# Optimization experiments

Hardware: AMD Instinct MI355X
Metric: run time of the kernel (lower is better)

The kernel has to match this reference:

```python
import jax, jax.numpy as jnp
import numpy as np

N_NODES = 50000
N_INC = 300000
IN_DIM = 256
OUT_DIM = 256
NEG_SLOPE = 0.2
BN_EPS = 1e-5


def setup_inputs() -> dict:
    key = jax.random.key(0)
    ks = jax.random.split(key, 8)
    x = jax.random.normal(ks[0], (N_NODES, IN_DIM), dtype=jnp.float32)
    node_idx = jax.random.randint(ks[1], (N_INC,), 0, N_NODES)
    edge_idx = jax.random.randint(ks[2], (N_INC,), 0, 20000)
    W = jax.random.normal(ks[3], (IN_DIM, OUT_DIM), dtype=jnp.float32) / np.sqrt(IN_DIM)
    att = jax.random.normal(ks[4], (2 * OUT_DIM,), dtype=jnp.float32) * 0.1
    bias = jnp.zeros((OUT_DIM,), dtype=jnp.float32)
    gamma = jnp.ones((OUT_DIM,), dtype=jnp.float32)
    beta = jnp.zeros((OUT_DIM,), dtype=jnp.float32)
    return {
        'x': x, 'node_idx': node_idx, 'edge_idx': edge_idx,
        'num_hyperedges': 20000,
        'W': W, 'att': att, 'bias': bias, 'gamma': gamma, 'beta': beta,
    }


def reference(x, node_idx, edge_idx, num_hyperedges, W, att, bias, gamma, beta):
    N = x.shape[0]
    M = num_hyperedges
    xw = x @ W                                  # [N, D]

    # attention over incidences (old-PyG: edge feature := node feature at edge id)
    x_i = xw[node_idx]                          # [E, D]
    x_j = xw[edge_idx]                          # [E, D]
    alpha = jnp.sum(jnp.concatenate([x_i, x_j], axis=-1) * att, axis=-1)  # [E]
    alpha = jax.nn.leaky_relu(alpha, NEG_SLOPE)
    # segment softmax grouped by node index
    amax = jax.ops.segment_max(alpha, node_idx, num_segments=N)
    amax = jnp.where(jnp.isfinite(amax), amax, 0.0)
    e = jnp.exp(alpha - amax[node_idx])
    esum = jax.ops.segment_sum(e, node_idx, num_segments=N)
    alpha = e / (esum[node_idx] + 1e-16)        # [E]

    ones = jnp.ones_like(alpha)
    Dn = jax.ops.segment_sum(ones, node_idx, num_segments=N)   # node degree
    Dinv = jnp.where(Dn > 0, 1.0 / Dn, 0.0)
    Be = jax.ops.segment_sum(ones, edge_idx, num_segments=M)   # edge degree
    Binv = jnp.where(Be > 0, 1.0 / Be, 0.0)

    # stage 1: node -> hyperedge, norm = B at target edge
    msg1 = (Binv[edge_idx] * alpha)[:, None] * x_i              # [E, D]
    edge_feat = jax.ops.segment_sum(msg1, edge_idx, num_segments=M)  # [M, D]

    # stage 2: hyperedge -> node, norm = D at target node
    msg2 = (Dinv[node_idx] * alpha)[:, None] * edge_feat[edge_idx]   # [E, D]
    out = jax.ops.segment_sum(msg2, node_idx, num_segments=N) + bias  # [N, D]

    # BatchNorm1d (training: batch stats, biased variance) + ELU
    mu = jnp.mean(out, axis=0)
    var = jnp.mean((out - mu) ** 2, axis=0)
    out = gamma * (out - mu) * jax.lax.rsqrt(var + BN_EPS) + beta
    return jax.nn.elu(out)
```

## Files before the change

### kernel.cpp

```cpp
#include <hip/hip_runtime.h>

#define N_NODES 50000
#define N_INC   300000
#define DIM     256
#define M_EDGES 20000
#define NEG_SLOPE 0.2f
#define BN_EPS  1e-5f
#define EBLK 20
#define NBLK 49

typedef __attribute__((ext_vector_type(8))) short short8;
typedef __attribute__((ext_vector_type(4))) float f32x4;

__device__ __forceinline__ unsigned bf16rn(float f) {
    unsigned u = __float_as_uint(f);
    return (u + 0x7FFFu + ((u >> 16) & 1u)) >> 16;
}
__device__ __forceinline__ float4 unp4(uint2 p) {
    return make_float4(__uint_as_float(p.x << 16),
                       __uint_as_float(p.x & 0xFFFF0000u),
                       __uint_as_float(p.y << 16),
                       __uint_as_float(p.y & 0xFFFF0000u));
}

__global__ void wt_kernel(const float* __restrict__ W, ushort* __restrict__ WT)
{
    int i = blockIdx.x * 256 + threadIdx.x;
    int k = i >> 8, n = i & 255;
    WT[n * 256 + k] = (ushort)bf16rn(W[i]);
}

#define GBM 256
__global__ __launch_bounds__(512) void gemm_persist(
    const float* __restrict__ A, const ushort* __restrict__ WT,
    const float* __restrict__ att,
    ushort* __restrict__ xwb, float* __restrict__ s1, float* __restrict__ s2)
{
    __shared__ __align__(16) char Bs[131072];
    int tid = threadIdx.x;
    int lane = tid & 63, w = tid >> 6;

    #pragma unroll
    for (int i = 0; i < 16; ++i) {
        int flat = tid + 512 * i;
        int n = flat >> 5, kc = flat & 31;
        uint4 v = *(const uint4*)(WT + n * 256 + kc * 8);
        int off = n * 512 + ((kc * 16) ^ ((n & 7) << 4));
        *(uint4*)(Bs + off) = v;
    }
    __syncthreads();

    int row0 = blockIdx.x * GBM + w * 32;

    short8 afrag[2][8];
    #pragma unroll
    for (int j = 0; j < 8; ++j) {
        #pragma unroll
        for (int s = 0; s < 2; ++s) {
            int row = row0 + s * 16 + (lane & 15);
            float4 u0 = make_float4(0.f, 0.f, 0.f, 0.f), u1 = u0;
            if (row < N_NODES) {
                const float* p = A + (size_t)row * DIM + j * 32 + (lane >> 4) * 8;
                u0 = *(const float4*)p;
                u1 = *(const float4*)(p + 4);
            }
            uint4 q;
            q.x = bf16rn(u0.x) | (bf16rn(u0.y) << 16);
            q.y = bf16rn(u0.z) | (bf16rn(u0.w) << 16);
            q.z = bf16rn(u1.x) | (bf16rn(u1.y) << 16);
            q.w = bf16rn(u1.z) | (bf16rn(u1.w) << 16);
            afrag[s][j] = *(short8*)&q;
        }
    }

    float p1a[2][4] = {}, p2a[2][4] = {};
    #pragma unroll
    for (int ch = 0; ch < 2; ++ch) {
        f32x4 acc[2][8] = {};
        #pragma unroll
        for (int j = 0; j < 8; ++j) {
            int kb = j * 64 + (lane >> 4) * 16;
            #pragma unroll
            for (int c = 0; c < 8; ++c) {
                int col = ch * 128 + c * 16 + (lane & 15);
                short8 b = *(const short8*)(Bs + col * 512 + (kb ^ ((col & 7) << 4)));
                acc[0][c] = __builtin_amdgcn_mfma_f32_16x16x32_bf16(afrag[0][j], b, acc[0][c], 0, 0, 0);
                acc[1][c] = __builtin_amdgcn_mfma_f32_16x16x32_bf16(afrag[1][j], b, acc[1][c], 0, 0, 0);
            }
        }
        #pragma unroll
        for (int c = 0; c < 8; ++c) {
            int col = ch * 128 + c * 16 + (lane & 15);
            float a1 = att[col], a2 = att[DIM + col];
            #pragma unroll
            for (int s = 0; s < 2; ++s)
                #pragma unroll
                for (int r = 0; r < 4; ++r) {
                    int row = row0 + s * 16 + (lane >> 4) * 4 + r;
                    float v = acc[s][c][r];
                    if (row < N_NODES)
                        xwb[(size_t)row * DIM + col] = (ushort)bf16rn(v);
                    p1a[s][r] += v * a1;
                    p2a[s][r] += v * a2;
                }
        }
    }
    #pragma unroll
    for (int s = 0; s < 2; ++s)
        #pragma unroll
        for (int r = 0; r < 4; ++r) {
            float p1 = p1a[s][r], p2 = p2a[s][r];
            #pragma unroll
            for (int msk = 1; msk < 16; msk <<= 1) {
                p1 += __shfl_xor(p1, msk);
                p2 += __shfl_xor(p2, msk);
            }
            int row = row0 + s * 16 + (lane >> 4) * 4 + r;
            if ((lane & 15) == 0 && row < N_NODES) {
                s1[row] = p1;
                s2[row] = p2;
            }
        }
}

__global__ void alpha_kernel(
    const int* __restrict__ node_idx, const int* __restrict__ edge_idx,
    const float* __restrict__ s1, const float* __restrict__ s2,
    float* __restrict__ ealpha, float* __restrict__ esum,
    int* __restrict__ cnt_n, int* __restrict__ cnt_e)
{
    int e = blockIdx.x * blockDim.x + threadIdx.x;
    if (e >= N_INC) return;
    int n = node_idx[e], h = edge_idx[e];
    float a = s1[n] + s2[h];
    a = a > 0.f ? a : NEG_SLOPE * a;
    float ea = __expf(a);
    ealpha[e] = ea;
    atomicAdd(esum + n, ea);
    atomicAdd(cnt_n + n, 1);
    atomicAdd(cnt_e + h, 1);
}

__global__ __launch_bounds__(1024) void scan_partial(
    const int* __restrict__ cnt_e, int* __restrict__ start_e, int* __restrict__ totals_e,
    const int* __restrict__ cnt_n, int* __restrict__ start_n, int* __restrict__ totals_n)
{
    int b = blockIdx.x;
    const int* cnt; int* start; int* totals; int n; int cb;
    if (b < EBLK) { cnt = cnt_e; start = start_e; totals = totals_e; n = M_EDGES; cb = b; }
    else          { cnt = cnt_n; start = start_n; totals = totals_n; n = N_NODES; cb = b - EBLK; }
    int tid = threadIdx.x, lane = tid & 63, wid = tid >> 6;
    int i = cb * 1024 + tid;
    int v = (i < n) ? cnt[i] : 0;
    #pragma unroll
    for (int off = 1; off < 64; off <<= 1) {
        int t = __shfl_up(v, off);
        if (lane >= off) v += t;
    }
    __shared__ int wsum[16];
    if (lane == 63) wsum[wid] = v;
    __syncthreads();
    if (wid == 0 && lane < 16) {
        int s = wsum[lane];
        #pragma unroll
        for (int off = 1; off < 16; off <<= 1) {
            int t = __shfl_up(s, off);
            if (lane >= off) s += t;
        }
        wsum[lane] = s;
    }
    __syncthreads();
    if (wid > 0) v += wsum[wid - 1];
    if (i < n) start[i + 1] = v;
    if (tid == 1023) totals[cb] = v;
}

__global__ void scan_totals(
    const int* __restrict__ totals_e, int* __restrict__ boff_e,
    const int* __restrict__ totals_n, int* __restrict__ boff_n,
    int* __restrict__ start_e, int* __restrict__ start_n)
{
    int lane = threadIdx.x;
    int ve0 = (lane < EBLK) ? totals_e[lane] : 0;
    int ve = ve0;
    #pragma unroll
    for (int off = 1; off < 64; off <<= 1) {
        int t = __shfl_up(ve, off);
        if (lane >= off) ve += t;
    }
    if (lane < EBLK) boff_e[lane] = ve - ve0;
    int vn0 = (lane < NBLK) ? totals_n[lane] : 0;
    int vn = vn0;
    #pragma unroll
    for (int off = 1; off < 64; off <<= 1) {
        int t = __shfl_up(vn, off);
        if (lane >= off) vn += t;
    }
    if (lane < NBLK) boff_n[lane] = vn - vn0;
    if (lane == 0) { start_e[0] = 0; start_n[0] = 0; }
}

__global__ void scan_add(
    int* __restrict__ start_e, const int* __restrict__ boff_e,
    const int* __restrict__ cnt_e, int* __restrict__ cur_e,
    int* __restrict__ start_n, const int* __restrict__ boff_n,
    const int* __restrict__ cnt_n, int* __restrict__ cur_n,
    const float* __restrict__ esum, float* __restrict__ rnorm)
{
    int id = blockIdx.x * 256 + threadIdx.x;
    if (id < M_EDGES) {
        int s = start_e[id + 1] + boff_e[id >> 10];
        start_e[id + 1] = s;
        cur_e[id] = s - cnt_e[id];
    } else if (id < M_EDGES + N_NODES) {
        int j = id - M_EDGES;
        int s = start_n[j + 1] + boff_n[j >> 10];
        start_n[j + 1] = s;
        cur_n[j] = s - cnt_n[j];
        rnorm[j] = 1.f / (esum[j] + 1e-16f);
    }
}

__global__ void scatter_kernel(
    const int* __restrict__ node_idx, const int* __restrict__ edge_idx,
    const float* __restrict__ ealpha, const float* __restrict__ rnorm,
    int* __restrict__ cur_e, int* __restrict__ cur_n,
    int* __restrict__ list_e, int* __restrict__ list_n, float* __restrict__ an)
{
    int e = blockIdx.x * blockDim.x + threadIdx.x;
    if (e >= N_INC) return;
    int n = node_idx[e];
    int p = atomicAdd(cur_e + edge_idx[e], 1);
    list_e[p] = e;
    int q = atomicAdd(cur_n + n, 1);
    list_n[q] = e;
    an[e] = ealpha[e] * rnorm[n];
}

__global__ __launch_bounds__(256) void stage1_kernel(
    const ushort* __restrict__ xwb, const int* __restrict__ node_idx,
    const float* __restrict__ an, const int* __restrict__ start_e,
    const int* __restrict__ list_e, ushort* __restrict__ edge_feat)
{
    int h = blockIdx.x * 4 + (threadIdx.x >> 6);
    if (h >= M_EDGES) return;
    int lane = threadIdx.x & 63;
    int j0 = start_e[h], j1 = start_e[h + 1];
    float4 acc = make_float4(0.f, 0.f, 0.f, 0.f);
    float4 ac2 = make_float4(0.f, 0.f, 0.f, 0.f);
    for (int base = j0; base < j1; base += 64) {
        int cnt = min(64, j1 - base);
        float wv = 0.f; int nv = 0;
        if (lane < cnt) { int e = list_e[base + lane]; wv = an[e]; nv = node_idx[e]; }
        int jj = 0;
        for (; jj + 4 <= cnt; jj += 4) {
            float wg0 = __shfl(wv, jj);     int n0 = __shfl(nv, jj);
            float wg1 = __shfl(wv, jj + 1); int n1 = __shfl(nv, jj + 1);
            float wg2 = __shfl(wv, jj + 2); int n2 = __shfl(nv, jj + 2);
            float wg3 = __shfl(wv, jj + 3); int n3 = __shfl(nv, jj + 3);
            uint2 p0 = *(const uint2*)(xwb + (size_t)n0 * DIM + lane * 4);
            uint2 p1 = *(const uint2*)(xwb + (size_t)n1 * DIM + lane * 4);
            uint2 p2 = *(const uint2*)(xwb + (size_t)n2 * DIM + lane * 4);
            uint2 p3 = *(const uint2*)(xwb + (size_t)n3 * DIM + lane * 4);
            float4 v0 = unp4(p0), v1 = unp4(p1), v2 = unp4(p2), v3 = unp4(p3);
            acc.x += wg0 * v0.x + wg1 * v1.x;  ac2.x += wg2 * v2.x + wg3 * v3.x;
            acc.y += wg0 * v0.y + wg1 * v1.y;  ac2.y += wg2 * v2.y + wg3 * v3.y;
            acc.z += wg0 * v0.z + wg1 * v1.z;  ac2.z += wg2 * v2.z + wg3 * v3.z;
            acc.w += wg0 * v0.w + wg1 * v1.w;  ac2.w += wg2 * v2.w + wg3 * v3.w;
        }
        for (; jj < cnt; ++jj) {
            float wg = __shfl(wv, jj); int n0 = __shfl(nv, jj);
            float4 v = unp4(*(const uint2*)(xwb + (size_t)n0 * DIM + lane * 4));
            acc.x += wg * v.x; acc.y += wg * v.y;
            acc.z += wg * v.z; acc.w += wg * v.w;
        }
    }
    acc.x += ac2.x; acc.y += ac2.y; acc.z += ac2.z; acc.w += ac2.w;
    float binv = (j1 > j0) ? 1.f / (float)(j1 - j0) : 0.f;
    uint2 p;
    p.x = bf16rn(acc.x * binv) | (bf16rn(acc.y * binv) << 16);
    p.y = bf16rn(acc.z * binv) | (bf16rn(acc.w * binv) << 16);
    *(uint2*)(edge_feat + (size_t)h * DIM + lane * 4) = p;
}

__global__ __launch_bounds__(256) void stage2_kernel(
    const ushort* __restrict__ edge_feat, const int* __restrict__ edge_idx,
    const float* __restrict__ an, const int* __restrict__ start_n,
    const int* __restrict__ list_n, const float* __restrict__ bias,
    float* __restrict__ out)
{
    int n = blockIdx.x * 4 + (threadIdx.x >> 6);
    if (n >= N_NODES) return;
    int lane = threadIdx.x & 63;
    int j0 = start_n[n], j1 = start_n[n + 1];
    float4 acc = make_float4(0.f, 0.f, 0.f, 0.f);
    float4 ac2 = make_float4(0.f, 0.f, 0.f, 0.f);
    for (int base = j0; base < j1; base += 64) {
        int cnt = min(64, j1 - base);
        float wv = 0.f; int hv = 0;
        if (lane < cnt) { int e = list_n[base + lane]; wv = an[e]; hv = edge_idx[e]; }
        int jj = 0;
        for (; jj + 4 <= cnt; jj += 4) {
            float wg0 = __shfl(wv, jj);     int h0 = __shfl(hv, jj);
            float wg1 = __shfl(wv, jj + 1); int h1 = __shfl(hv, jj + 1);
            float wg2 = __shfl(wv, jj + 2); int h2 = __shfl(hv, jj + 2);
            float wg3 = __shfl(wv, jj + 3); int h3 = __shfl(hv, jj + 3);
            uint2 p0 = *(const uint2*)(edge_feat + (size_t)h0 * DIM + lane * 4);
            uint2 p1 = *(const uint2*)(edge_feat + (size_t)h1 * DIM + lane * 4);
            uint2 p2 = *(const uint2*)(edge_feat + (size_t)h2 * DIM + lane * 4);
            uint2 p3 = *(const uint2*)(edge_feat + (size_t)h3 * DIM + lane * 4);
            float4 v0 = unp4(p0), v1 = unp4(p1), v2 = unp4(p2), v3 = unp4(p3);
            acc.x += wg0 * v0.x + wg1 * v1.x;  ac2.x += wg2 * v2.x + wg3 * v3.x;
            acc.y += wg0 * v0.y + wg1 * v1.y;  ac2.y += wg2 * v2.y + wg3 * v3.y;
            acc.z += wg0 * v0.z + wg1 * v1.z;  ac2.z += wg2 * v2.z + wg3 * v3.z;
            acc.w += wg0 * v0.w + wg1 * v1.w;  ac2.w += wg2 * v2.w + wg3 * v3.w;
        }
        for (; jj < cnt; ++jj) {
            float wg = __shfl(wv, jj); int h0 = __shfl(hv, jj);
            float4 v = unp4(*(const uint2*)(edge_feat + (size_t)h0 * DIM + lane * 4));
            acc.x += wg * v.x; acc.y += wg * v.y;
            acc.z += wg * v.z; acc.w += wg * v.w;
        }
    }
    acc.x += ac2.x; acc.y += ac2.y; acc.z += ac2.z; acc.w += ac2.w;
    float dinv = (j1 > j0) ? 1.f / (float)(j1 - j0) : 0.f;
    float4 b = *(const float4*)(bias + lane * 4);
    acc.x = fmaf(acc.x, dinv, b.x); acc.y = fmaf(acc.y, dinv, b.y);
    acc.z = fmaf(acc.z, dinv, b.z); acc.w = fmaf(acc.w, dinv, b.w);
    *(float4*)(out + (size_t)n * DIM + lane * 4) = acc;
}

__global__ __launch_bounds__(256) void stats_kernel(
    const float* __restrict__ out, float* __restrict__ stats)
{
    __shared__ float lsum[4][256], lsq[4][256];
    int tid = threadIdx.x, lane = tid & 63, w = tid >> 6;
    int c4 = lane * 4;
    int rows_per = (N_NODES + gridDim.x - 1) / gridDim.x;
    int r0 = blockIdx.x * rows_per;
    int r1 = min(r0 + rows_per, N_NODES);
    float4 s = make_float4(0.f, 0.f, 0.f, 0.f);
    float4 q = make_float4(0.f, 0.f, 0.f, 0.f);
    for (int r = r0 + w; r < r1; r += 4) {
        float4 v = *(const float4*)(out + (size_t)r * DIM + c4);
        s.x += v.x; s.y += v.y; s.z += v.z; s.w += v.w;
        q.x += v.x * v.x; q.y += v.y * v.y; q.z += v.z * v.z; q.w += v.w * v.w;
    }
    *(float4*)&lsum[w][c4] = s;
    *(float4*)&lsq[w][c4] = q;
    __syncthreads();
    if (w == 0) {
        #pragma unroll
        for (int i = 1; i < 4; ++i) {
            s.x += lsum[i][c4]; s.y += lsum[i][c4 + 1]; s.z += lsum[i][c4 + 2]; s.w += lsum[i][c4 + 3];
            q.x += lsq[i][c4];  q.y += lsq[i][c4 + 1];  q.z += lsq[i][c4 + 2];  q.w += lsq[i][c4 + 3];
        }
        atomicAdd(stats + c4 + 0, s.x); atomicAdd(stats + c4 + 1, s.y);
        atomicAdd(stats + c4 + 2, s.z); atomicAdd(stats + c4 + 3, s.w);
        atomicAdd(stats + DIM + c4 + 0, q.x); atomicAdd(stats + DIM + c4 + 1, q.y);
        atomicAdd(stats + DIM + c4 + 2, q.z); atomicAdd(stats + DIM + c4 + 3, q.w);
    }
}

__global__ void bnprep_kernel(
    const float* __restrict__ stats, const float* __restrict__ gamma,
    const float* __restrict__ beta, float* __restrict__ scale, float* __restrict__ shift)
{
    int c = threadIdx.x;
    float mu = stats[c] * (1.f / N_NODES);
    float var = stats[DIM + c] * (1.f / N_NODES) - mu * mu;
    float sc = gamma[c] * rsqrtf(var + BN_EPS);
    scale[c] = sc;
    shift[c] = beta[c] - mu * sc;
}

__global__ __launch_bounds__(256) void bn_kernel(
    float* __restrict__ out, const float* __restrict__ scale, const float* __restrict__ shift)
{
    int idx = blockIdx.x * 256 + threadIdx.x;
    int c4 = (idx & 63) * 4;
    float4 sc = *(const float4*)(scale + c4);
    float4 sh = *(const float4*)(shift + c4);
    float4 v = ((float4*)out)[idx];
    v.x = fmaf(v.x, sc.x, sh.x); v.y = fmaf(v.y, sc.y, sh.y);
    v.z = fmaf(v.z, sc.z, sh.z); v.w = fmaf(v.w, sc.w, sh.w);
    v.x = v.x > 0.f ? v.x : __expf(v.x) - 1.f;
    v.y = v.y > 0.f ? v.y : __expf(v.y) - 1.f;
    v.z = v.z > 0.f ? v.z : __expf(v.z) - 1.f;
    v.w = v.w > 0.f ? v.w : __expf(v.w) - 1.f;
    ((float4*)out)[idx] = v;
}

extern "C" void kernel_launch(void* const* d_in, const int* in_sizes, int n_in,
                              void* d_out, int out_size, void* d_ws, size_t ws_size,
                              hipStream_t stream)
{
    const float* x        = (const float*)d_in[0];
    const int*   node_idx = (const int*)d_in[1];
    const int*   edge_idx = (const int*)d_in[2];
    const float* W        = (const float*)d_in[4];
    const float* att      = (const float*)d_in[5];
    const float* bias     = (const float*)d_in[6];
    const float* gamma    = (const float*)d_in[7];
    const float* beta     = (const float*)d_in[8];
    float* out = (float*)d_out;
    ushort* xwb = (ushort*)d_out;

    ushort* edge_feat = (ushort*)d_ws;
    int*   cnt_e   = (int*)(edge_feat + (size_t)M_EDGES * DIM);
    int*   cnt_n   = cnt_e + M_EDGES;
    float* stats   = (float*)(cnt_n + N_NODES);
    float* esum    = stats + 2 * DIM;
    float* s1      = esum + N_NODES;
    float* s2      = s1 + N_NODES;
    float* ealpha  = s2 + N_NODES;
    float* an      = ealpha + N_INC;
    float* rnorm   = an + N_INC;
    int*   start_e = (int*)(rnorm + N_NODES);
    int*   start_n = start_e + M_EDGES + 1;
    int*   cur_e   = start_n + N_NODES + 1;
    int*   cur_n   = cur_e + M_EDGES;
    int*   list_e  = cur_n + N_NODES;
    int*   list_n  = list_e + N_INC;
    ushort* WT     = (ushort*)(list_n + N_INC);
    int*   totals_e = (int*)(WT + 256 * 256);
    int*   boff_e   = totals_e + EBLK;
    int*   totals_n = boff_e + EBLK;
    int*   boff_n   = totals_n + NBLK;
    float* scale    = (float*)(boff_n + NBLK);
    float* shift    = scale + DIM;

    hipMemsetAsync(cnt_e, 0,
        (size_t)(M_EDGES + N_NODES + 2 * DIM + N_NODES) * 4, stream);

    wt_kernel<<<256, 256, 0, stream>>>(W, WT);
    gemm_persist<<<(N_NODES + GBM - 1) / GBM, 512, 0, stream>>>(x, WT, att, xwb, s1, s2);
    alpha_kernel<<<(N_INC + 255) / 256, 256, 0, stream>>>(node_idx, edge_idx, s1, s2, ealpha, esum, cnt_n, cnt_e);
    scan_partial<<<EBLK + NBLK, 1024, 0, stream>>>(cnt_e, start_e, totals_e, cnt_n, start_n, totals_n);
    scan_totals<<<1, 64, 0, stream>>>(totals_e, boff_e, totals_n, boff_n, start_e, start_n);
    scan_add<<<(M_EDGES + N_NODES + 255) / 256, 256, 0, stream>>>(
        start_e, boff_e, cnt_e, cur_e, start_n, boff_n, cnt_n, cur_n, esum, rnorm);
    scatter_kernel<<<(N_INC + 255) / 256, 256, 0, stream>>>(node_idx, edge_idx, ealpha, rnorm, cur_e, cur_n, list_e, list_n, an);
    stage1_kernel<<<(M_EDGES + 3) / 4, 256, 0, stream>>>(xwb, node_idx, an, start_e, list_e, edge_feat);
    stage2_kernel<<<(N_NODES + 3) / 4, 256, 0, stream>>>(edge_feat, edge_idx, an, start_n, list_n, bias, out);
    stats_kernel<<<128, 256, 0, stream>>>(out, stats);
    bnprep_kernel<<<1, 256, 0, stream>>>(stats, gamma, beta, scale, shift);
    bn_kernel<<<N_NODES * DIM / 4 / 256, 256, 0, stream>>>(out, scale, shift);
}
```

Measured before the change: 236.2 us.

## Build CSR lists from atomic ranks and drop float atomics for softmax sums

The counting pass now records each incidence's rank within its node and edge bucket, packed into one word. The scatter pass can then place entries directly without a second round of atomics. The float atomicAdd for the softmax denominator is replaced by a per-node reduction over the CSR list in a new small kernel. The softmax normalisation is folded into the stage kernels: stage1 applies it per gathered incidence and stage2 applies it once per output row. This removes atomics and the precomputed per-incidence weight array, at the cost of an extra launch, an extra gather in stage1, and a 16-bit limit on ranks. That limit is fine for these degrees.

```diff
diff --git a/kernel.cpp b/kernel.cpp
--- a/kernel.cpp
+++ b/kernel.cpp
@@ -123,10 +123,10 @@
         }
 }
 
-__global__ void alpha_kernel(
+__global__ void rank_kernel(
     const int* __restrict__ node_idx, const int* __restrict__ edge_idx,
     const float* __restrict__ s1, const float* __restrict__ s2,
-    float* __restrict__ ealpha, float* __restrict__ esum,
+    float* __restrict__ ealpha, unsigned* __restrict__ rank_pk,
     int* __restrict__ cnt_n, int* __restrict__ cnt_e)
 {
     int e = blockIdx.x * blockDim.x + threadIdx.x;
@@ -134,11 +134,10 @@
     int n = node_idx[e], h = edge_idx[e];
     float a = s1[n] + s2[h];
     a = a > 0.f ? a : NEG_SLOPE * a;
-    float ea = __expf(a);
-    ealpha[e] = ea;
-    atomicAdd(esum + n, ea);
-    atomicAdd(cnt_n + n, 1);
-    atomicAdd(cnt_e + h, 1);
+    ealpha[e] = __expf(a);
+    unsigned rn = (unsigned)atomicAdd(cnt_n + n, 1);
+    unsigned re = (unsigned)atomicAdd(cnt_e + h, 1);
+    rank_pk[e] = (re << 16) | rn;
 }
 
 __global__ __launch_bounds__(1024) void scan_partial(
@@ -202,45 +201,46 @@
 
 __global__ void scan_add(
     int* __restrict__ start_e, const int* __restrict__ boff_e,
-    const int* __restrict__ cnt_e, int* __restrict__ cur_e,
-    int* __restrict__ start_n, const int* __restrict__ boff_n,
-    const int* __restrict__ cnt_n, int* __restrict__ cur_n,
-    const float* __restrict__ esum, float* __restrict__ rnorm)
+    int* __restrict__ start_n, const int* __restrict__ boff_n)
 {
     int id = blockIdx.x * 256 + threadIdx.x;
-    if (id < M_EDGES) {
-        int s = start_e[id + 1] + boff_e[id >> 10];
-        start_e[id + 1] = s;
-        cur_e[id] = s - cnt_e[id];
-    } else if (id < M_EDGES + N_NODES) {
+    if (id < M_EDGES) start_e[id + 1] += boff_e[id >> 10];
+    else if (id < M_EDGES + N_NODES) {
         int j = id - M_EDGES;
-        int s = start_n[j + 1] + boff_n[j >> 10];
-        start_n[j + 1] = s;
-        cur_n[j] = s - cnt_n[j];
-        rnorm[j] = 1.f / (esum[j] + 1e-16f);
-    }
-}
-
-__global__ void scatter_kernel(
+        start_n[j + 1] += boff_n[j >> 10];
+    }
+}
+
+__global__ void place_kernel(
     const int* __restrict__ node_idx, const int* __restrict__ edge_idx,
-    const float* __restrict__ ealpha, const float* __restrict__ rnorm,
-    int* __restrict__ cur_e, int* __restrict__ cur_n,
-    int* __restrict__ list_e, int* __restrict__ list_n, float* __restrict__ an)
+    const unsigned* __restrict__ rank_pk,
+    const int* __restrict__ start_e, const int* __restrict__ start_n,
+    int* __restrict__ list_e, int* __restrict__ list_n)
 {
     int e = blockIdx.x * blockDim.x + threadIdx.x;
     if (e >= N_INC) return;
-    int n = node_idx[e];
-    int p = atomicAdd(cur_e + edge_idx[e], 1);
-    list_e[p] = e;
-    int q = atomicAdd(cur_n + n, 1);
-    list_n[q] = e;
-    an[e] = ealpha[e] * rnorm[n];
+    unsigned pk = rank_pk[e];
+    list_e[start_e[edge_idx[e]] + (pk >> 16)] = e;
+    list_n[start_n[node_idx[e]] + (pk & 0xFFFFu)] = e;
+}
+
+__global__ void rnorm_kernel(
+    const float* __restrict__ ealpha, const int* __restrict__ start_n,
+    const int* __restrict__ list_n, float* __restrict__ rnorm)
+{
+    int n = blockIdx.x * blockDim.x + threadIdx.x;
+    if (n >= N_NODES) return;
+    int j0 = start_n[n], j1 = start_n[n + 1];
+    float s = 0.f;
+    for (int j = j0; j < j1; ++j) s += ealpha[list_n[j]];
+    rnorm[n] = 1.f / (s + 1e-16f);
 }
 
 __global__ __launch_bounds__(256) void stage1_kernel(
     const ushort* __restrict__ xwb, const int* __restrict__ node_idx,
-    const float* __restrict__ an, const int* __restrict__ start_e,
-    const int* __restrict__ list_e, ushort* __restrict__ edge_feat)
+    const float* __restrict__ ealpha, const float* __restrict__ rnorm,
+    const int* __restrict__ start_e, const int* __restrict__ list_e,
+    ushort* __restrict__ edge_feat)
 {
     int h = blockIdx.x * 4 + (threadIdx.x >> 6);
     if (h >= M_EDGES) return;
@@ -251,7 +251,12 @@
     for (int base = j0; base < j1; base += 64) {
         int cnt = min(64, j1 - base);
         float wv = 0.f; int nv = 0;
-        if (lane < cnt) { int e = list_e[base + lane]; wv = an[e]; nv = node_idx[e]; }
+        if (lane < cnt) {
+            int e = list_e[base + lane];
+            int n_ = node_idx[e];
+            wv = ealpha[e] * rnorm[n_];
+            nv = n_;
+        }
         int jj = 0;
         for (; jj + 4 <= cnt; jj += 4) {
             float wg0 = __shfl(wv, jj);     int n0 = __shfl(nv, jj);
@@ -285,9 +290,9 @@
 
 __global__ __launch_bounds__(256) void stage2_kernel(
     const ushort* __restrict__ edge_feat, const int* __restrict__ edge_idx,
-    const float* __restrict__ an, const int* __restrict__ start_n,
-    const int* __restrict__ list_n, const float* __restrict__ bias,
-    float* __restrict__ out)
+    const float* __restrict__ ealpha, const float* __restrict__ rnorm,
+    const int* __restrict__ start_n, const int* __restrict__ list_n,
+    const float* __restrict__ bias, float* __restrict__ out)
 {
     int n = blockIdx.x * 4 + (threadIdx.x >> 6);
     if (n >= N_NODES) return;
@@ -298,7 +303,7 @@
     for (int base = j0; base < j1; base += 64) {
         int cnt = min(64, j1 - base);
         float wv = 0.f; int hv = 0;
-        if (lane < cnt) { int e = list_n[base + lane]; wv = an[e]; hv = edge_idx[e]; }
+        if (lane < cnt) { int e = list_n[base + lane]; wv = ealpha[e]; hv = edge_idx[e]; }
         int jj = 0;
         for (; jj + 4 <= cnt; jj += 4) {
             float wg0 = __shfl(wv, jj);     int h0 = __shfl(hv, jj);
@@ -323,10 +328,10 @@
         }
     }
     acc.x += ac2.x; acc.y += ac2.y; acc.z += ac2.z; acc.w += ac2.w;
-    float dinv = (j1 > j0) ? 1.f / (float)(j1 - j0) : 0.f;
+    float sc = (j1 > j0) ? rnorm[n] / (float)(j1 - j0) : 0.f;
     float4 b = *(const float4*)(bias + lane * 4);
-    acc.x = fmaf(acc.x, dinv, b.x); acc.y = fmaf(acc.y, dinv, b.y);
-    acc.z = fmaf(acc.z, dinv, b.z); acc.w = fmaf(acc.w, dinv, b.w);
+    acc.x = fmaf(acc.x, sc, b.x); acc.y = fmaf(acc.y, sc, b.y);
+    acc.z = fmaf(acc.z, sc, b.z); acc.w = fmaf(acc.w, sc, b.w);
     *(float4*)(out + (size_t)n * DIM + lane * 4) = acc;
 }
 
@@ -410,17 +415,14 @@
     int*   cnt_e   = (int*)(edge_feat + (size_t)M_EDGES * DIM);
     int*   cnt_n   = cnt_e + M_EDGES;
     float* stats   = (float*)(cnt_n + N_NODES);
-    float* esum    = stats + 2 * DIM;
-    float* s1      = esum + N_NODES;
+    float* s1      = stats + 2 * DIM;
     float* s2      = s1 + N_NODES;
     float* ealpha  = s2 + N_NODES;
-    float* an      = ealpha + N_INC;
-    float* rnorm   = an + N_INC;
+    unsigned* rank_pk = (unsigned*)(ealpha + N_INC);
+    float* rnorm   = (float*)(rank_pk + N_INC);
     int*   start_e = (int*)(rnorm + N_NODES);
     int*   start_n = start_e + M_EDGES + 1;
-    int*   cur_e   = start_n + N_NODES + 1;
-    int*   cur_n   = cur_e + M_EDGES;
-    int*   list_e  = cur_n + N_NODES;
+    int*   list_e  = start_n + N_NODES + 1;
     int*   list_n  = list_e + N_INC;
     ushort* WT     = (ushort*)(list_n + N_INC);
     int*   totals_e = (int*)(WT + 256 * 256);
@@ -430,19 +432,18 @@
     float* scale    = (float*)(boff_n + NBLK);
     float* shift    = scale + DIM;
 
-    hipMemsetAsync(cnt_e, 0,
-        (size_t)(M_EDGES + N_NODES + 2 * DIM + N_NODES) * 4, stream);
+    hipMemsetAsync(cnt_e, 0, (size_t)(M_EDGES + N_NODES + 2 * DIM) * 4, stream);
 
     wt_kernel<<<256, 256, 0, stream>>>(W, WT);
     gemm_persist<<<(N_NODES + GBM - 1) / GBM, 512, 0, stream>>>(x, WT, att, xwb, s1, s2);
-    alpha_kernel<<<(N_INC + 255) / 256, 256, 0, stream>>>(node_idx, edge_idx, s1, s2, ealpha, esum, cnt_n, cnt_e);
+    rank_kernel<<<(N_INC + 255) / 256, 256, 0, stream>>>(node_idx, edge_idx, s1, s2, ealpha, rank_pk, cnt_n, cnt_e);
     scan_partial<<<EBLK + NBLK, 1024, 0, stream>>>(cnt_e, start_e, totals_e, cnt_n, start_n, totals_n);
     scan_totals<<<1, 64, 0, stream>>>(totals_e, boff_e, totals_n, boff_n, start_e, start_n);
-    scan_add<<<(M_EDGES + N_NODES + 255) / 256, 256, 0, stream>>>(
-        start_e, boff_e, cnt_e, cur_e, start_n, boff_n, cnt_n, cur_n, esum, rnorm);
-    scatter_kernel<<<(N_INC + 255) / 256, 256, 0, stream>>>(node_idx, edge_idx, ealpha, rnorm, cur_e, cur_n, list_e, list_n, an);
-    stage1_kernel<<<(M_EDGES + 3) / 4, 256, 0, stream>>>(xwb, node_idx, an, start_e, list_e, edge_feat);
-    stage2_kernel<<<(N_NODES + 3) / 4, 256, 0, stream>>>(edge_feat, edge_idx, an, start_n, list_n, bias, out);
+    scan_add<<<(M_EDGES + N_NODES + 255) / 256, 256, 0, stream>>>(start_e, boff_e, start_n, boff_n);
+    place_kernel<<<(N_INC + 255) / 256, 256, 0, stream>>>(node_idx, edge_idx, rank_pk, start_e, start_n, list_e, list_n);
+    rnorm_kernel<<<(N_NODES + 255) / 256, 256, 0, stream>>>(ealpha, start_n, list_n, rnorm);
+    stage1_kernel<<<(M_EDGES + 3) / 4, 256, 0, stream>>>(xwb, node_idx, ealpha, rnorm, start_e, list_e, edge_feat);
+    stage2_kernel<<<(N_NODES + 3) / 4, 256, 0, stream>>>(edge_feat, edge_idx, ealpha, rnorm, start_n, list_n, bias, out);
     stats_kernel<<<128, 256, 0, stream>>>(out, stats);
     bnprep_kernel<<<1, 256, 0, stream>>>(stats, gamma, beta, scale, shift);
     bn_kernel<<<N_NODES * DIM / 4 / 256, 256, 0, stream>>>(out, scale, shift);
```

Result: faster. 207.4 us (-12.2%).
